# Performance work log

Hardware: AMD Instinct MI355X
Metric: run time of the kernel (lower is better)

## Reference

```python
import jax, jax.numpy as jnp
import numpy as np

B, N, D = 8, 2048, 512

def setup_inputs() -> dict:
    key = jax.random.key(0)
    k1, k2, k3, k4, k5 = jax.random.split(key, 5)
    s = 1.0 / np.sqrt(D)
    return {
        "x": jax.random.normal(k1, (B, N, D), dtype=jnp.float32),
        "w_qkv": jax.random.normal(k2, (D, 3 * D), dtype=jnp.float32) * s,
        "b_qkv": jax.random.normal(k3, (3 * D,), dtype=jnp.float32) * 0.01,
        "w_fc": jax.random.normal(k4, (D, D), dtype=jnp.float32) * s,
        "b_fc": jax.random.normal(k5, (D,), dtype=jnp.float32) * 0.01,
    }

def reference(x, w_qkv, b_qkv, w_fc, b_fc):
    scale = 1.0 / (x.shape[-1] ** 0.5)
    qkv = x @ w_qkv + b_qkv                      # [B, N, 3D]
    q, k, v = jnp.split(qkv, 3, axis=-1)         # each [B, N, D]
    attn = jnp.einsum("bnd,bmd->bnm", q, k) * scale
    attn = jax.nn.softmax(attn, axis=-1)
    out = jnp.einsum("bnm,bmd->bnd", attn, v)
    return out @ w_fc + b_fc + x
```

## Files before the change

kernel.cpp:

```cpp
#include <hip/hip_runtime.h>
#include <stdint.h>

typedef unsigned short u16;
typedef unsigned int u32;
typedef __attribute__((ext_vector_type(8))) short short8;
typedef __attribute__((ext_vector_type(4))) float f32x4;
typedef __attribute__((ext_vector_type(8))) unsigned short u16x8;
typedef __attribute__((ext_vector_type(4))) float float4_t;

__device__ __forceinline__ float b2f(u16 u) { return __uint_as_float(((u32)u) << 16); }
__device__ __forceinline__ u16 f2b(float f) {
  u32 u = __float_as_uint(f);
  u += 0x7fffu + ((u >> 16) & 1u);
  return (u16)(u >> 16);
}

typedef const __attribute__((address_space(1))) void* gas_t;
typedef __attribute__((address_space(3))) void* las_t;
__device__ __forceinline__ void gl_lds16(const void* g, void* l) {
  __builtin_amdgcn_global_load_lds((gas_t)(uintptr_t)g, (las_t)(u32)(uintptr_t)l, 16, 0, 0);
}
__device__ __forceinline__ void barrier_pin() {
  __builtin_amdgcn_sched_barrier(0);
  __builtin_amdgcn_s_barrier();
  __builtin_amdgcn_sched_barrier(0);
}
__device__ __forceinline__ void lgkm0_pin() {
  asm volatile("s_waitcnt lgkmcnt(0)" ::: "memory");
  __builtin_amdgcn_sched_barrier(0);
}

__global__ __launch_bounds__(256) void cvt_f2b_kernel(const float* __restrict__ src,
                                                      u16* __restrict__ dst, long n) {
  long i = ((long)blockIdx.x * 256 + threadIdx.x) * 8;
  if (i >= n) return;
  float4_t v0 = *(const float4_t*)(src + i);
  float4_t v1 = *(const float4_t*)(src + i + 4);
  u16x8 o;
#pragma unroll
  for (int j = 0; j < 4; ++j) { o[j] = f2b(v0[j]); o[4 + j] = f2b(v1[j]); }
  *(u16x8*)(dst + i) = o;
}

__global__ __launch_bounds__(256) void tr_cvt(const float* __restrict__ src,
                                              u16* __restrict__ dst, int R, int C) {
  __shared__ float t[32][33];
  const int bx = blockIdx.x * 32;
  const int by = blockIdx.y * 32;
  const int tx = threadIdx.x & 31, ty = threadIdx.x >> 5;
#pragma unroll
  for (int i = 0; i < 32; i += 8)
    t[ty + i][tx] = src[(long)(by + ty + i) * C + bx + tx];
  __syncthreads();
#pragma unroll
  for (int i = 0; i < 32; i += 8)
    dst[(long)(bx + ty + i) * R + by + tx] = f2b(t[tx][ty + i]);
}

__global__ __launch_bounds__(256) void tr_v(const u16* __restrict__ qkv, u16* __restrict__ vt) {
  __shared__ u16 t[32][33];
  const int b = blockIdx.z;
  const int r0 = blockIdx.x * 32;
  const int d0 = blockIdx.y * 32;
  const int tx = threadIdx.x & 31, ty = threadIdx.x >> 5;
#pragma unroll
  for (int i = 0; i < 32; i += 8)
    t[ty + i][tx] = qkv[((long)b * 2048 + r0 + ty + i) * 1536 + 1024 + d0 + tx];
  __syncthreads();
#pragma unroll
  for (int i = 0; i < 32; i += 8)
    vt[((long)b * 512 + d0 + ty + i) * 2048 + r0 + tx] = t[tx][ty + i];
}

__global__ __launch_bounds__(256) void sum_inv(const float* __restrict__ part,
                                               float* __restrict__ inv_l) {
  const int r = blockIdx.x * 256 + threadIdx.x;
  const float* p = part + (long)r * 16;
  float s = 0.f;
#pragma unroll
  for (int i = 0; i < 16; ++i) s += p[i];
  inv_l[r] = 1.0f / s;
}

template <bool OUT_F32, bool BIAS, bool RES, bool EXPSUM, bool DIVL>
__global__ __launch_bounds__(512, 4)
void gemm128(const u16* __restrict__ A, const u16* __restrict__ Bt, void* __restrict__ Cv,
             const float* __restrict__ bias, const float* __restrict__ res,
             float* __restrict__ part, const float* __restrict__ inv_l,
             int K, int lda, int ldb, int ldc,
             long aStride, long bStride, long cStride, float alpha) {
  __shared__ u16 As[2][128 * 64];
  __shared__ u16 Bs[2][128 * 64];
  __shared__ float lsum[EXPSUM ? 4 : 1][EXPSUM ? 128 : 1];
  const int tid = threadIdx.x;
  const int wid = tid >> 6, lane = tid & 63;
  const int wr = wid >> 2, wc = wid & 3;
  const int lr = lane & 15, lg = lane >> 4;

  const int gx = gridDim.x, gy = gridDim.y;
  int id = (blockIdx.z * gy + blockIdx.y) * gx + blockIdx.x;
  const int nwg = gx * gy * gridDim.z;
  id = (id & 7) * (nwg >> 3) + (id >> 3);
  const int bxi = id % gx;
  const int t2 = id / gx;
  const int byi = t2 % gy;
  const long z = t2 / gy;

  A += z * aStride;
  Bt += z * bStride;
  const int by = byi * 128;
  const int bx = bxi * 128;

  f32x4 acc[4][2] = {};
  short8 ah[4][2], bh[2][2];

  const int w8l = wid * 8 + (lane >> 3);
  const int scol_src = ((lane & 7) ^ (lane >> 3)) * 8;
  const int scol_lin = (lane & 7) * 8;
  const int nT = K >> 6;
  const int sx = lane & 7;

  auto stage = [&](int kt) {
    const int bb = kt & 1;
    const long kc = (long)kt * 64 + scol_src;
#pragma unroll
    for (int r = 0; r < 2; ++r) {
      const int row = r * 64 + w8l;
      gl_lds16(A + (long)(by + row) * lda + kc, &As[bb][row * 64 + scol_lin]);
    }
#pragma unroll
    for (int r = 0; r < 2; ++r) {
      const int row = r * 64 + w8l;
      gl_lds16(Bt + (long)(bx + row) * ldb + kc, &Bs[bb][row * 64 + scol_lin]);
    }
  };

  stage(0);
  asm volatile("s_waitcnt vmcnt(0)" ::: "memory");
  barrier_pin();

  for (int T = 0; T < nT; ++T) {
    const int bb = T & 1;
    const bool more = (T + 1) < nT;
    if (more) stage(T + 1);
#pragma unroll
    for (int mi = 0; mi < 4; ++mi)
#pragma unroll
      for (int ks = 0; ks < 2; ++ks)
        ah[mi][ks] = *(const short8*)&As[bb][(wr * 64 + mi * 16 + lr) * 64 +
                                             (((ks * 4 + lg) ^ sx) * 8)];
#pragma unroll
    for (int n = 0; n < 2; ++n)
#pragma unroll
      for (int ks = 0; ks < 2; ++ks)
        bh[n][ks] = *(const short8*)&Bs[bb][(wc * 32 + n * 16 + lr) * 64 +
                                            (((ks * 4 + lg) ^ sx) * 8)];
    lgkm0_pin();
    __builtin_amdgcn_s_setprio(1);
#pragma unroll
    for (int mi = 0; mi < 4; ++mi)
#pragma unroll
      for (int n = 0; n < 2; ++n)
#pragma unroll
        for (int ks = 0; ks < 2; ++ks)
          acc[mi][n] = __builtin_amdgcn_mfma_f32_16x16x32_bf16(
              ah[mi][ks], bh[n][ks], acc[mi][n], 0, 0, 0);
    __builtin_amdgcn_s_setprio(0);
    if (more) asm volatile("s_waitcnt vmcnt(0)" ::: "memory");
    barrier_pin();
  }

  if constexpr (EXPSUM) {
    u16* C = (u16*)Cv + z * cStride;
#pragma unroll
    for (int mi = 0; mi < 4; ++mi) {
#pragma unroll
      for (int j = 0; j < 4; ++j) {
        const long row = by + wr * 64 + mi * 16 + lg * 4 + j;
        float e0 = __expf(acc[mi][0][j] * alpha);
        float e1 = __expf(acc[mi][1][j] * alpha);
        C[row * (long)ldc + bx + wc * 32 + 0 * 16 + lr] = f2b(e0);
        C[row * (long)ldc + bx + wc * 32 + 1 * 16 + lr] = f2b(e1);
        float t = e0 + e1;
#pragma unroll
        for (int off = 1; off < 16; off <<= 1) t += __shfl_xor(t, off);
        if (lr == 0) lsum[wc][wr * 64 + mi * 16 + lg * 4 + j] = t;
      }
    }
    __syncthreads();
    if (tid < 128) {
      const float s = lsum[0][tid] + lsum[1][tid] + lsum[2][tid] + lsum[3][tid];
      part[(z * 2048 + by + tid) * 16 + bxi] = s;
    }
  } else if constexpr (OUT_F32) {
    float* C = (float*)Cv + z * cStride;
#pragma unroll
    for (int mi = 0; mi < 4; ++mi)
#pragma unroll
      for (int ni = 0; ni < 2; ++ni)
#pragma unroll
        for (int j = 0; j < 4; ++j) {
          const long row = by + wr * 64 + mi * 16 + lg * 4 + j;
          const int col = bx + wc * 32 + ni * 16 + lr;
          float v = acc[mi][ni][j] * alpha;
          if (BIAS) v += bias[col];
          if (RES) v += res[row * (long)ldc + col];
          C[row * (long)ldc + col] = v;
        }
  } else {
    u16* C = (u16*)Cv + z * cStride;
#pragma unroll
    for (int mi = 0; mi < 4; ++mi)
#pragma unroll
      for (int ni = 0; ni < 2; ++ni)
#pragma unroll
        for (int j = 0; j < 4; ++j) {
          const long row = by + wr * 64 + mi * 16 + lg * 4 + j;
          const int col = bx + wc * 32 + ni * 16 + lr;
          float v = acc[mi][ni][j] * alpha;
          if (DIVL) v *= inv_l[z * 2048 + by + wr * 64 + mi * 16 + lg * 4 + j];
          if (BIAS) v += bias[col];
          C[row * (long)ldc + col] = f2b(v);
        }
  }
}

extern "C" void kernel_launch(void* const* d_in, const int* in_sizes, int n_in,
                              void* d_out, int out_size, void* d_ws, size_t ws_size,
                              hipStream_t stream) {
  const float* x = (const float*)d_in[0];
  const float* w_qkv = (const float*)d_in[1];
  const float* b_qkv = (const float*)d_in[2];
  const float* w_fc = (const float*)d_in[3];
  const float* b_fc = (const float*)d_in[4];
  float* out = (float*)d_out;

  char* ws = (char*)d_ws;
  const long MT = 16384;
  u16* xb = (u16*)(ws);
  u16* wqkvT = (u16*)(ws + 16777216);
  u16* wfcT = (u16*)(ws + 18350080);
  u16* qkv = (u16*)(ws + 18874368);
  u16* vt = (u16*)(ws + 69206016);
  u16* S = (u16*)(ws + 85983232);
  u16* attn = xb;
  float* part = (float*)(ws + 16777216);
  float* inv_l = (float*)(ws + 16777216 + 1048576);

  cvt_f2b_kernel<<<4096, 256, 0, stream>>>(x, xb, MT * 512);
  tr_cvt<<<dim3(48, 16), 256, 0, stream>>>(w_qkv, wqkvT, 512, 1536);
  tr_cvt<<<dim3(16, 16), 256, 0, stream>>>(w_fc, wfcT, 512, 512);

  gemm128<false, true, false, false, false><<<dim3(12, 128, 1), 512, 0, stream>>>(
      xb, wqkvT, qkv, b_qkv, nullptr, nullptr, nullptr,
      512, 512, 512, 1536, 0, 0, 0, 1.0f);

  tr_v<<<dim3(64, 16, 8), 256, 0, stream>>>(qkv, vt);

  gemm128<false, false, false, true, false><<<dim3(16, 16, 8), 512, 0, stream>>>(
      qkv, qkv + 512, S, nullptr, nullptr, part, nullptr,
      512, 1536, 1536, 2048,
      (long)2048 * 1536, (long)2048 * 1536, (long)2048 * 2048, 0.04419417382415922f);

  sum_inv<<<64, 256, 0, stream>>>(part, inv_l);

  gemm128<false, false, false, false, true><<<dim3(4, 16, 8), 512, 0, stream>>>(
      S, vt, attn, nullptr, nullptr, nullptr, inv_l,
      2048, 2048, 2048, 512,
      (long)2048 * 2048, (long)512 * 2048, (long)2048 * 512, 1.0f);

  gemm128<true, true, true, false, false><<<dim3(4, 128, 1), 512, 0, stream>>>(
      attn, wfcT, out, b_fc, x, nullptr, nullptr,
      512, 512, 512, 512, 0, 0, 0, 1.0f);
}
```

Measured before the change: 173.2 us.

## Compute softmax row sums via ones-MFMA inside PV GEMM, drop sum_inv kernel

After: 163.6 us. 5.5% less time.

```diff
diff --git a/kernel.cpp b/kernel.cpp
--- a/kernel.cpp
+++ b/kernel.cpp
@@ -72,26 +72,15 @@
     vt[((long)b * 512 + d0 + ty + i) * 2048 + r0 + tx] = t[tx][ty + i];
 }
 
-__global__ __launch_bounds__(256) void sum_inv(const float* __restrict__ part,
-                                               float* __restrict__ inv_l) {
-  const int r = blockIdx.x * 256 + threadIdx.x;
-  const float* p = part + (long)r * 16;
-  float s = 0.f;
-#pragma unroll
-  for (int i = 0; i < 16; ++i) s += p[i];
-  inv_l[r] = 1.0f / s;
-}
-
-template <bool OUT_F32, bool BIAS, bool RES, bool EXPSUM, bool DIVL>
+template <bool OUT_F32, bool BIAS, bool RES, bool EXP_EPI, bool ROWSUM_DIV>
 __global__ __launch_bounds__(512, 4)
 void gemm128(const u16* __restrict__ A, const u16* __restrict__ Bt, void* __restrict__ Cv,
              const float* __restrict__ bias, const float* __restrict__ res,
-             float* __restrict__ part, const float* __restrict__ inv_l,
              int K, int lda, int ldb, int ldc,
              long aStride, long bStride, long cStride, float alpha) {
   __shared__ u16 As[2][128 * 64];
   __shared__ u16 Bs[2][128 * 64];
-  __shared__ float lsum[EXPSUM ? 4 : 1][EXPSUM ? 128 : 1];
+  __shared__ float lsum[ROWSUM_DIV ? 128 : 1];
   const int tid = threadIdx.x;
   const int wid = tid >> 6, lane = tid & 63;
   const int wr = wid >> 2, wc = wid & 3;
@@ -112,7 +101,11 @@
   const int bx = bxi * 128;
 
   f32x4 acc[4][2] = {};
+  f32x4 acc_l[4] = {};
   short8 ah[4][2], bh[2][2];
+  short8 ones;
+#pragma unroll
+  for (int j = 0; j < 8; ++j) ones[j] = (short)0x3F80;
 
   const int w8l = wid * 8 + (lane >> 3);
   const int scol_src = ((lane & 7) ^ (lane >> 3)) * 8;
@@ -165,33 +158,44 @@
         for (int ks = 0; ks < 2; ++ks)
           acc[mi][n] = __builtin_amdgcn_mfma_f32_16x16x32_bf16(
               ah[mi][ks], bh[n][ks], acc[mi][n], 0, 0, 0);
+    if constexpr (ROWSUM_DIV) {
+      if (wc == 0) {
+#pragma unroll
+        for (int mi = 0; mi < 4; ++mi)
+#pragma unroll
+          for (int ks = 0; ks < 2; ++ks)
+            acc_l[mi] = __builtin_amdgcn_mfma_f32_16x16x32_bf16(
+                ah[mi][ks], ones, acc_l[mi], 0, 0, 0);
+      }
+    }
     __builtin_amdgcn_s_setprio(0);
     if (more) asm volatile("s_waitcnt vmcnt(0)" ::: "memory");
     barrier_pin();
   }
 
-  if constexpr (EXPSUM) {
+  if constexpr (ROWSUM_DIV) {
+    if (wc == 0 && lr == 0) {
+#pragma unroll
+      for (int mi = 0; mi < 4; ++mi)
+#pragma unroll
+        for (int j = 0; j < 4; ++j)
+          lsum[wr * 64 + mi * 16 + lg * 4 + j] = acc_l[mi][j];
+    }
+    __syncthreads();
+  }
+
+  if constexpr (EXP_EPI) {
     u16* C = (u16*)Cv + z * cStride;
 #pragma unroll
-    for (int mi = 0; mi < 4; ++mi) {
-#pragma unroll
-      for (int j = 0; j < 4; ++j) {
-        const long row = by + wr * 64 + mi * 16 + lg * 4 + j;
-        float e0 = __expf(acc[mi][0][j] * alpha);
-        float e1 = __expf(acc[mi][1][j] * alpha);
-        C[row * (long)ldc + bx + wc * 32 + 0 * 16 + lr] = f2b(e0);
-        C[row * (long)ldc + bx + wc * 32 + 1 * 16 + lr] = f2b(e1);
-        float t = e0 + e1;
-#pragma unroll
-        for (int off = 1; off < 16; off <<= 1) t += __shfl_xor(t, off);
-        if (lr == 0) lsum[wc][wr * 64 + mi * 16 + lg * 4 + j] = t;
-      }
-    }
-    __syncthreads();
-    if (tid < 128) {
-      const float s = lsum[0][tid] + lsum[1][tid] + lsum[2][tid] + lsum[3][tid];
-      part[(z * 2048 + by + tid) * 16 + bxi] = s;
-    }
+    for (int mi = 0; mi < 4; ++mi)
+#pragma unroll
+      for (int ni = 0; ni < 2; ++ni)
+#pragma unroll
+        for (int j = 0; j < 4; ++j) {
+          const long row = by + wr * 64 + mi * 16 + lg * 4 + j;
+          const int col = bx + wc * 32 + ni * 16 + lr;
+          C[row * (long)ldc + col] = f2b(__expf(acc[mi][ni][j] * alpha));
+        }
   } else if constexpr (OUT_F32) {
     float* C = (float*)Cv + z * cStride;
 #pragma unroll
@@ -212,16 +216,19 @@
 #pragma unroll
     for (int mi = 0; mi < 4; ++mi)
 #pragma unroll
-      for (int ni = 0; ni < 2; ++ni)
-#pragma unroll
-        for (int j = 0; j < 4; ++j) {
+      for (int j = 0; j < 4; ++j) {
+        float invl = 1.0f;
+        if constexpr (ROWSUM_DIV) invl = 1.0f / lsum[wr * 64 + mi * 16 + lg * 4 + j];
+#pragma unroll
+        for (int ni = 0; ni < 2; ++ni) {
           const long row = by + wr * 64 + mi * 16 + lg * 4 + j;
           const int col = bx + wc * 32 + ni * 16 + lr;
           float v = acc[mi][ni][j] * alpha;
-          if (DIVL) v *= inv_l[z * 2048 + by + wr * 64 + mi * 16 + lg * 4 + j];
+          if constexpr (ROWSUM_DIV) v *= invl;
           if (BIAS) v += bias[col];
           C[row * (long)ldc + col] = f2b(v);
         }
+      }
   }
 }
 
@@ -244,32 +251,28 @@
   u16* vt = (u16*)(ws + 69206016);
   u16* S = (u16*)(ws + 85983232);
   u16* attn = xb;
-  float* part = (float*)(ws + 16777216);
-  float* inv_l = (float*)(ws + 16777216 + 1048576);
 
   cvt_f2b_kernel<<<4096, 256, 0, stream>>>(x, xb, MT * 512);
   tr_cvt<<<dim3(48, 16), 256, 0, stream>>>(w_qkv, wqkvT, 512, 1536);
   tr_cvt<<<dim3(16, 16), 256, 0, stream>>>(w_fc, wfcT, 512, 512);
 
   gemm128<false, true, false, false, false><<<dim3(12, 128, 1), 512, 0, stream>>>(
-      xb, wqkvT, qkv, b_qkv, nullptr, nullptr, nullptr,
+      xb, wqkvT, qkv, b_qkv, nullptr,
       512, 512, 512, 1536, 0, 0, 0, 1.0f);
 
   tr_v<<<dim3(64, 16, 8), 256, 0, stream>>>(qkv, vt);
 
   gemm128<false, false, false, true, false><<<dim3(16, 16, 8), 512, 0, stream>>>(
-      qkv, qkv + 512, S, nullptr, nullptr, part, nullptr,
+      qkv, qkv + 512, S, nullptr, nullptr,
       512, 1536, 1536, 2048,
       (long)2048 * 1536, (long)2048 * 1536, (long)2048 * 2048, 0.04419417382415922f);
 
-  sum_inv<<<64, 256, 0, stream>>>(part, inv_l);
-
   gemm128<false, false, false, false, true><<<dim3(4, 16, 8), 512, 0, stream>>>(
-      S, vt, attn, nullptr, nullptr, nullptr, inv_l,
+      S, vt, attn, nullptr, nullptr,
       2048, 2048, 2048, 512,
       (long)2048 * 2048, (long)512 * 2048, (long)2048 * 512, 1.0f);
 
   gemm128<true, true, true, false, false><<<dim3(4, 128, 1), 512, 0, stream>>>(
-      attn, wfcT, out, b_fc, x, nullptr, nullptr,
+      attn, wfcT, out, b_fc, x,
       512, 512, 512, 512, 0, 0, 0, 1.0f);
 }
```
